# Optimization experiments

Hardware: AMD Instinct MI355X
Metric: run time of the kernel (lower is better)

The kernel has to match this reference:

```python
import jax, jax.numpy as jnp
import numpy as np

NUM_EXPERTS = 8
HIDDEN = 2048
INTER = 4096
TOKENS = 8192  # divisible by NUM_EXPERTS


def setup_inputs() -> dict:
    key = jax.random.key(0)
    k1, k2, k3 = jax.random.split(key, 3)
    hidden_states = jax.random.normal(k1, (TOKENS, HIDDEN), dtype=jnp.float32)
    gate_up_proj = jax.random.normal(k2, (NUM_EXPERTS, HIDDEN, 2 * INTER), dtype=jnp.float32) * 0.02
    down_proj = jax.random.normal(k3, (NUM_EXPERTS, INTER, HIDDEN), dtype=jnp.float32) * 0.02
    return {"hidden_states": hidden_states, "gate_up_proj": gate_up_proj, "down_proj": down_proj}


def reference(hidden_states, gate_up_proj, down_proj):
    E, H = gate_up_proj.shape[0], gate_up_proj.shape[1]
    x = hidden_states.reshape(E, -1, H)                      # (E, T/E, H)
    gate_up = jnp.einsum('eth,ehf->etf', x, gate_up_proj)    # (E, T/E, 2I)
    gate, up = jnp.split(gate_up, 2, axis=-1)
    acted = up * jax.nn.silu(gate)                           # (E, T/E, I)
    out = jnp.einsum('eti,eih->eth', acted, down_proj)       # (E, T/E, H)
    return out.reshape(-1, H)
```

## Files before the change

### kernel.cpp

```cpp
#include <hip/hip_runtime.h>


#define E_   8
#define H_   2048
#define I_   4096
#define T_   8192
#define TPE  1024

typedef __bf16 bf16x8 __attribute__((ext_vector_type(8)));
typedef float  f32x4  __attribute__((ext_vector_type(4)));

__device__ __forceinline__ unsigned short f2bf(float f) {
  union { float f; unsigned int u; } v; v.f = f;
  unsigned int u = v.u;
  u += 0x7FFFu + ((u >> 16) & 1u);
  return (unsigned short)(u >> 16);
}

__device__ __forceinline__ void async16(const void* g, void* l) {
  __builtin_amdgcn_global_load_lds(
      (__attribute__((address_space(1))) void*)(g),
      (__attribute__((address_space(3))) void*)(l), 16, 0, 0);
}

__global__ void convert_bf16(const float* __restrict__ src,
                             unsigned short* __restrict__ dst, long n) {
  long i = ((long)blockIdx.x * blockDim.x + threadIdx.x) * 4;
  const long stride = (long)gridDim.x * blockDim.x * 4;
  for (; i < n; i += stride) {
    const float4 v = *(const float4*)&src[i];
    ushort4 o;
    o.x = f2bf(v.x); o.y = f2bf(v.y); o.z = f2bf(v.z); o.w = f2bf(v.w);
    *(ushort4*)&dst[i] = o;
  }
}

__global__ void transpose_bf16(const float* __restrict__ src,
                               unsigned short* __restrict__ dst,
                               int K, int N) {
  __shared__ float tile[32][33];
  const long base = (long)blockIdx.z * (long)K * (long)N;
  src += base; dst += base;
  const int n0 = blockIdx.x * 32, k0 = blockIdx.y * 32;
  const int r  = threadIdx.x >> 3;
  const int c4 = (threadIdx.x & 7) * 4;

  const float4 v = *(const float4*)&src[(long)(k0 + r) * N + n0 + c4];
  tile[r][c4 + 0] = v.x; tile[r][c4 + 1] = v.y;
  tile[r][c4 + 2] = v.z; tile[r][c4 + 3] = v.w;
  __syncthreads();

  ushort4 o;
  o.x = f2bf(tile[c4 + 0][r]);
  o.y = f2bf(tile[c4 + 1][r]);
  o.z = f2bf(tile[c4 + 2][r]);
  o.w = f2bf(tile[c4 + 3][r]);
  *(ushort4*)&dst[(long)(n0 + r) * K + k0 + c4] = o;
}

__global__ void transpose_w1_perm(const float* __restrict__ src,
                                  unsigned short* __restrict__ dst) {
  __shared__ float tile[32][33];
  const long sbase = (long)blockIdx.z * (long)H_ * (2 * I_);
  const long dbase = (long)blockIdx.z * (long)(2 * I_) * H_;
  const int n0 = blockIdx.x * 32, k0 = blockIdx.y * 32;
  const int r  = threadIdx.x >> 3;
  const int c4 = (threadIdx.x & 7) * 4;

  const float4 v = *(const float4*)&src[sbase + (long)(k0 + r) * (2 * I_) + n0 + c4];
  tile[r][c4 + 0] = v.x; tile[r][c4 + 1] = v.y;
  tile[r][c4 + 2] = v.z; tile[r][c4 + 3] = v.w;
  __syncthreads();

  const int n = n0 + r;
  int np;
  if (n < I_) np = ((n >> 4) << 5) + (n & 15);
  else { const int j = n - I_; np = ((j >> 4) << 5) + 16 + (j & 15); }

  ushort4 o;
  o.x = f2bf(tile[c4 + 0][r]);
  o.y = f2bf(tile[c4 + 1][r]);
  o.z = f2bf(tile[c4 + 2][r]);
  o.w = f2bf(tile[c4 + 3][r]);
  *(ushort4*)&dst[dbase + (long)np * H_ + k0 + c4] = o;
}

template <int K, int NBN, bool SILU>
__global__ __launch_bounds__(512, 2)
void gemm_8ph(const unsigned short* __restrict__ Aall,
              const unsigned short* __restrict__ Ball,
              void* __restrict__ Cout,
              long sA, long sB, long sC) {
  extern __shared__ char smem[];
  constexpr int NT = K / 64;

  const int tid  = threadIdx.x;
  const int wave = tid >> 6;
  const int lane = tid & 63;
  const int lr   = lane & 15;
  const int lq   = lane >> 4;
  const int wid_m = wave >> 2;
  const int wid_n = wave & 3;

  const int nwg = gridDim.x;
  const int bid = blockIdx.x;
  const int wg  = (bid & 7) * (nwg >> 3) + (bid >> 3);
  const int mb  = wg & 3;
  const int tmp = wg >> 2;
  const int nb  = tmp % NBN;
  const int e   = tmp / NBN;

  const unsigned short* A = Aall + (long)e * sA + (long)(mb * 256) * K;
  const unsigned short* B = Ball + (long)e * sB + (long)(nb * 256) * K;

  const int stl  = tid >> 3;
  const int scol = ((tid & 7) ^ (stl & 7)) * 8;

  auto stageA = [&](int bi, int q, int kt) {
    const long col = (long)kt * 64 + scol;
    char* l0 = smem + bi * 32768 + q * 16384 + wave * 1024;
    async16(A + (long)(q * 64 + stl) * K + col,        l0);
    async16(A + (long)(128 + q * 64 + stl) * K + col,  l0 + 8192);
  };
  auto stageB = [&](int bi, int u, int kt) {
    const long col = (long)kt * 64 + scol;
    char* l0 = smem + 65536 + bi * 32768 + u * 16384 + wave * 1024;
    const int low = stl & 31;
    const int w0  = stl >> 5;
    async16(B + (long)((w0) * 64 + u * 32 + low) * K + col,     l0);
    async16(B + (long)((2 + w0) * 64 + u * 32 + low) * K + col, l0 + 8192);
  };

  const int ax0 = ((0 + lq) ^ (lr & 7)) * 16;
  const int ax1 = ((4 + lq) ^ (lr & 7)) * 16;

  f32x4 acc[8][4];
#pragma unroll
  for (int m = 0; m < 8; ++m)
#pragma unroll
    for (int n = 0; n < 4; ++n) acc[m][n] = (f32x4)0.0f;

  stageA(0, 0, 0);
  stageB(0, 1, 0);
  stageA(0, 1, 0);
  stageB(0, 0, 0);
  stageA(1, 0, NT > 1 ? 1 : 0);
  stageB(1, 1, NT > 1 ? 1 : 0);
  stageA(1, 1, NT > 1 ? 1 : 0);
  asm volatile("s_waitcnt vmcnt(6)" ::: "memory");
  __builtin_amdgcn_s_barrier();

#pragma unroll 1
  for (int t = 0; t < NT; ++t) {
    const int cur = t & 1;
    const char* LA = smem + cur * 32768;
    const char* LB = smem + 65536 + cur * 32768;
    const int t1v = (t + 1 < NT) ? t + 1 : NT - 1;
    const int t2v = (t + 2 < NT) ? t + 2 : NT - 1;
    const int bo  = cur ^ 1;

    bf16x8 a[4][2], b0[2][2], b1[2][2];

#pragma unroll
    for (int mf = 0; mf < 4; ++mf) {
      const int st = wid_m * 64 + mf * 16 + lr;
      a[mf][0] = *(const bf16x8*)(LA + st * 128 + ax0);
      a[mf][1] = *(const bf16x8*)(LA + st * 128 + ax1);
    }
#pragma unroll
    for (int nf = 0; nf < 2; ++nf) {
      const int st = wid_n * 32 + nf * 16 + lr;
      b0[nf][0] = *(const bf16x8*)(LB + st * 128 + ax0);
      b0[nf][1] = *(const bf16x8*)(LB + st * 128 + ax1);
    }
    stageB(bo, 0, t1v);
    __builtin_amdgcn_s_barrier();
    asm volatile("s_waitcnt lgkmcnt(0)" ::: "memory");
    __builtin_amdgcn_s_setprio(1);
#pragma unroll
    for (int mf = 0; mf < 4; ++mf)
#pragma unroll
      for (int nf = 0; nf < 2; ++nf) {
        acc[mf][nf] = __builtin_amdgcn_mfma_f32_16x16x32_bf16(a[mf][0], b0[nf][0], acc[mf][nf], 0, 0, 0);
        acc[mf][nf] = __builtin_amdgcn_mfma_f32_16x16x32_bf16(a[mf][1], b0[nf][1], acc[mf][nf], 0, 0, 0);
      }
    __builtin_amdgcn_s_setprio(0);
    __builtin_amdgcn_s_barrier();

#pragma unroll
    for (int nf = 0; nf < 2; ++nf) {
      const int st = 128 + wid_n * 32 + nf * 16 + lr;
      b1[nf][0] = *(const bf16x8*)(LB + st * 128 + ax0);
      b1[nf][1] = *(const bf16x8*)(LB + st * 128 + ax1);
    }
    stageA(cur, 0, t2v);
    __builtin_amdgcn_s_barrier();
    asm volatile("s_waitcnt lgkmcnt(0)" ::: "memory");
    __builtin_amdgcn_s_setprio(1);
#pragma unroll
    for (int mf = 0; mf < 4; ++mf)
#pragma unroll
      for (int nf = 0; nf < 2; ++nf) {
        acc[mf][2 + nf] = __builtin_amdgcn_mfma_f32_16x16x32_bf16(a[mf][0], b1[nf][0], acc[mf][2 + nf], 0, 0, 0);
        acc[mf][2 + nf] = __builtin_amdgcn_mfma_f32_16x16x32_bf16(a[mf][1], b1[nf][1], acc[mf][2 + nf], 0, 0, 0);
      }
    __builtin_amdgcn_s_setprio(0);
    __builtin_amdgcn_s_barrier();

#pragma unroll
    for (int mf = 0; mf < 4; ++mf) {
      const int st = 128 + wid_m * 64 + mf * 16 + lr;
      a[mf][0] = *(const bf16x8*)(LA + st * 128 + ax0);
      a[mf][1] = *(const bf16x8*)(LA + st * 128 + ax1);
    }
    stageB(cur, 1, t2v);
    __builtin_amdgcn_s_barrier();
    asm volatile("s_waitcnt lgkmcnt(0)" ::: "memory");
    __builtin_amdgcn_s_setprio(1);
#pragma unroll
    for (int mf = 0; mf < 4; ++mf)
#pragma unroll
      for (int nf = 0; nf < 2; ++nf) {
        acc[4 + mf][2 + nf] = __builtin_amdgcn_mfma_f32_16x16x32_bf16(a[mf][0], b1[nf][0], acc[4 + mf][2 + nf], 0, 0, 0);
        acc[4 + mf][2 + nf] = __builtin_amdgcn_mfma_f32_16x16x32_bf16(a[mf][1], b1[nf][1], acc[4 + mf][2 + nf], 0, 0, 0);
      }
    __builtin_amdgcn_s_setprio(0);
    __builtin_amdgcn_s_barrier();

    stageA(cur, 1, t2v);
    asm volatile("s_waitcnt vmcnt(6)" ::: "memory");
    __builtin_amdgcn_s_barrier();
    asm volatile("s_waitcnt lgkmcnt(0)" ::: "memory");
    __builtin_amdgcn_s_setprio(1);
#pragma unroll
    for (int mf = 0; mf < 4; ++mf)
#pragma unroll
      for (int nf = 0; nf < 2; ++nf) {
        acc[4 + mf][nf] = __builtin_amdgcn_mfma_f32_16x16x32_bf16(a[mf][0], b0[nf][0], acc[4 + mf][nf], 0, 0, 0);
        acc[4 + mf][nf] = __builtin_amdgcn_mfma_f32_16x16x32_bf16(a[mf][1], b0[nf][1], acc[4 + mf][nf], 0, 0, 0);
      }
    __builtin_amdgcn_s_setprio(0);
    __builtin_amdgcn_s_barrier();
  }

  if (SILU) {
    unsigned short* Cc = (unsigned short*)Cout + (long)e * sC;
    const int colbase = nb * 128 + wid_n * 32;
#pragma unroll
    for (int mf = 0; mf < 8; ++mf)
#pragma unroll
      for (int nfp = 0; nfp < 2; ++nfp)
#pragma unroll
        for (int rr = 0; rr < 4; ++rr) {
          const int row = mb * 256 + wid_m * 128 + mf * 16 + lq * 4 + rr;
          const int col = colbase + nfp * 16 + lr;
          const float g = acc[mf][nfp * 2][rr];
          const float u = acc[mf][nfp * 2 + 1][rr];
          Cc[(long)row * I_ + col] = f2bf(u * (g / (1.0f + __expf(-g))));
        }
  } else {
    float* Cc = (float*)Cout + (long)e * sC;
    const int colbase = nb * 256 + wid_n * 64;
#pragma unroll
    for (int mf = 0; mf < 8; ++mf)
#pragma unroll
      for (int nf = 0; nf < 4; ++nf)
#pragma unroll
        for (int rr = 0; rr < 4; ++rr) {
          const int row = mb * 256 + wid_m * 128 + mf * 16 + lq * 4 + rr;
          const int col = colbase + nf * 16 + lr;
          Cc[(long)row * H_ + col] = acc[mf][nf][rr];
        }
  }
}

extern "C" void kernel_launch(void* const* d_in, const int* in_sizes, int n_in,
                              void* d_out, int out_size, void* d_ws, size_t ws_size,
                              hipStream_t stream) {
  const float* hs = (const float*)d_in[0];
  const float* w1 = (const float*)d_in[1];
  const float* w2 = (const float*)d_in[2];
  float* out = (float*)d_out;
  char* ws = (char*)d_ws;

  const long HB_B  = (long)T_ * H_ * 2;
  const long ACT_B = (long)T_ * I_ * 2;
  const long W1T_B = (long)E_ * 2 * I_ * H_ * 2;
  const long W2T_B = (long)E_ * H_ * I_ * 2;
  if (ws_size < (size_t)(HB_B + ACT_B + W1T_B + W2T_B)) return;

  unsigned short* hiddenB = (unsigned short*)(ws);
  unsigned short* acted   = (unsigned short*)(ws + HB_B);
  unsigned short* W1t     = (unsigned short*)(ws + HB_B + ACT_B);
  unsigned short* W2t     = (unsigned short*)(ws + HB_B + ACT_B + W1T_B);

  hipLaunchKernelGGL(convert_bf16, dim3(2048), dim3(256), 0, stream,
                     hs, hiddenB, (long)T_ * H_);
  hipLaunchKernelGGL(transpose_w1_perm, dim3((2 * I_) / 32, H_ / 32, E_), dim3(256), 0, stream,
                     w1, W1t);
  hipLaunchKernelGGL(transpose_bf16, dim3(H_ / 32, I_ / 32, E_), dim3(256), 0, stream,
                     w2, W2t, I_, H_);

  hipLaunchKernelGGL((gemm_8ph<H_, 32, true>), dim3(1024), dim3(512), 131072, stream,
                     hiddenB, W1t, acted,
                     (long)TPE * H_, (long)2 * I_ * H_, (long)TPE * I_);
  hipLaunchKernelGGL((gemm_8ph<I_, 8, false>), dim3(256), dim3(512), 131072, stream,
                     acted, W2t, out,
                     (long)TPE * I_, (long)H_ * I_, (long)TPE * H_);
}
```

Measured before the change: 620.2 us.

## Fuse fp32 weight transpose and bf16 conversion into GEMM B-operand staging

Removes the separate weight transpose/convert kernels and their bf16 workspace. Each GEMM now reads fp32 weights straight from the original layout through registers, converts them to bf16 and writes the swizzled tile to LDS, with the gate/up interleave folded into the column mapping. This saves a full read and write pass over the large weight tensors. The cost is strided scalar global loads (one float per k-row per thread) in place of 16-byte async loads, plus more register and VALU work inside the main loop.

```diff
diff --git a/kernel.cpp b/kernel.cpp
--- a/kernel.cpp
+++ b/kernel.cpp
@@ -22,6 +22,11 @@
       (__attribute__((address_space(1))) void*)(g),
       (__attribute__((address_space(3))) void*)(l), 16, 0, 0);
 }
+
+#define SB0()    __builtin_amdgcn_sched_barrier(0)
+#define BAR()    __builtin_amdgcn_s_barrier()
+#define WAITLGKM() asm volatile("s_waitcnt lgkmcnt(0)" ::: "memory")
+#define WAITVM(n)  asm volatile("s_waitcnt vmcnt(" #n ")" ::: "memory")
 
 __global__ void convert_bf16(const float* __restrict__ src,
                              unsigned short* __restrict__ dst, long n) {
@@ -35,62 +40,12 @@
   }
 }
 
-__global__ void transpose_bf16(const float* __restrict__ src,
-                               unsigned short* __restrict__ dst,
-                               int K, int N) {
-  __shared__ float tile[32][33];
-  const long base = (long)blockIdx.z * (long)K * (long)N;
-  src += base; dst += base;
-  const int n0 = blockIdx.x * 32, k0 = blockIdx.y * 32;
-  const int r  = threadIdx.x >> 3;
-  const int c4 = (threadIdx.x & 7) * 4;
-
-  const float4 v = *(const float4*)&src[(long)(k0 + r) * N + n0 + c4];
-  tile[r][c4 + 0] = v.x; tile[r][c4 + 1] = v.y;
-  tile[r][c4 + 2] = v.z; tile[r][c4 + 3] = v.w;
-  __syncthreads();
-
-  ushort4 o;
-  o.x = f2bf(tile[c4 + 0][r]);
-  o.y = f2bf(tile[c4 + 1][r]);
-  o.z = f2bf(tile[c4 + 2][r]);
-  o.w = f2bf(tile[c4 + 3][r]);
-  *(ushort4*)&dst[(long)(n0 + r) * K + k0 + c4] = o;
-}
-
-__global__ void transpose_w1_perm(const float* __restrict__ src,
-                                  unsigned short* __restrict__ dst) {
-  __shared__ float tile[32][33];
-  const long sbase = (long)blockIdx.z * (long)H_ * (2 * I_);
-  const long dbase = (long)blockIdx.z * (long)(2 * I_) * H_;
-  const int n0 = blockIdx.x * 32, k0 = blockIdx.y * 32;
-  const int r  = threadIdx.x >> 3;
-  const int c4 = (threadIdx.x & 7) * 4;
-
-  const float4 v = *(const float4*)&src[sbase + (long)(k0 + r) * (2 * I_) + n0 + c4];
-  tile[r][c4 + 0] = v.x; tile[r][c4 + 1] = v.y;
-  tile[r][c4 + 2] = v.z; tile[r][c4 + 3] = v.w;
-  __syncthreads();
-
-  const int n = n0 + r;
-  int np;
-  if (n < I_) np = ((n >> 4) << 5) + (n & 15);
-  else { const int j = n - I_; np = ((j >> 4) << 5) + 16 + (j & 15); }
-
-  ushort4 o;
-  o.x = f2bf(tile[c4 + 0][r]);
-  o.y = f2bf(tile[c4 + 1][r]);
-  o.z = f2bf(tile[c4 + 2][r]);
-  o.w = f2bf(tile[c4 + 3][r]);
-  *(ushort4*)&dst[dbase + (long)np * H_ + k0 + c4] = o;
-}
-
-template <int K, int NBN, bool SILU>
+template <int K, int NBN, int LDB, bool SILU>
 __global__ __launch_bounds__(512, 2)
-void gemm_8ph(const unsigned short* __restrict__ Aall,
-              const unsigned short* __restrict__ Ball,
-              void* __restrict__ Cout,
-              long sA, long sB, long sC) {
+void gemm_fused(const unsigned short* __restrict__ Aall,
+                const float* __restrict__ Ball,
+                void* __restrict__ Cout,
+                long sA, long sB, long sC) {
   extern __shared__ char smem[];
   constexpr int NT = K / 64;
 
@@ -111,7 +66,7 @@
   const int e   = tmp / NBN;
 
   const unsigned short* A = Aall + (long)e * sA + (long)(mb * 256) * K;
-  const unsigned short* B = Ball + (long)e * sB + (long)(nb * 256) * K;
+  const float*          B = Ball + (long)e * sB;
 
   const int stl  = tid >> 3;
   const int scol = ((tid & 7) ^ (stl & 7)) * 8;
@@ -122,13 +77,46 @@
     async16(A + (long)(q * 64 + stl) * K + col,        l0);
     async16(A + (long)(128 + q * 64 + stl) * K + col,  l0 + 8192);
   };
-  auto stageB = [&](int bi, int u, int kt) {
-    const long col = (long)kt * 64 + scol;
-    char* l0 = smem + 65536 + bi * 32768 + u * 16384 + wave * 1024;
-    const int low = stl & 31;
-    const int w0  = stl >> 5;
-    async16(B + (long)((w0) * 64 + u * 32 + low) * K + col,     l0);
-    async16(B + (long)((2 + w0) * 64 + u * 32 + low) * K + col, l0 + 8192);
+
+  const int stB = tid & 255;
+  int colg;
+  {
+    const int b  = stB >> 7;
+    const int r  = stB & 127;
+    const int w  = r >> 5;
+    const int nf = (r >> 4) & 1;
+    const int l4 = stB & 15;
+    if (SILU) {
+      const int c = w * 32 + b * 16 + l4;
+      colg = nb * 128 + c + (nf ? I_ : 0);
+    } else {
+      colg = nb * 256 + w * 64 + (b * 2 + nf) * 16 + l4;
+    }
+  }
+  const float* Bp = B + colg;
+  const int koB = tid >> 8;
+
+  float bv[16];
+  auto loadB = [&](int g, int kt) {
+#pragma unroll
+    for (int uu = 0; uu < 2; ++uu) {
+      const int ko = (g * 2 + uu) * 2 + koB;
+      const long krow = (long)kt * 64 + ko * 8;
+#pragma unroll
+      for (int j = 0; j < 8; ++j)
+        bv[uu * 8 + j] = Bp[(krow + j) * (long)LDB];
+    }
+  };
+  auto writeB = [&](int bo, int g) {
+    char* LB = smem + 65536 + bo * 32768;
+#pragma unroll
+    for (int uu = 0; uu < 2; ++uu) {
+      const int ko = (g * 2 + uu) * 2 + koB;
+      bf16x8 pk;
+#pragma unroll
+      for (int j = 0; j < 8; ++j) pk[j] = (__bf16)bv[uu * 8 + j];
+      *(bf16x8*)(LB + stB * 128 + ((ko ^ (stB & 7)) * 16)) = pk;
+    }
   };
 
   const int ax0 = ((0 + lq) ^ (lr & 7)) * 16;
@@ -140,24 +128,30 @@
 #pragma unroll
     for (int n = 0; n < 4; ++n) acc[m][n] = (f32x4)0.0f;
 
+  const int t1p = (NT > 1) ? 1 : 0;
+  loadB(0, 0);
   stageA(0, 0, 0);
-  stageB(0, 1, 0);
   stageA(0, 1, 0);
-  stageB(0, 0, 0);
-  stageA(1, 0, NT > 1 ? 1 : 0);
-  stageB(1, 1, NT > 1 ? 1 : 0);
-  stageA(1, 1, NT > 1 ? 1 : 0);
-  asm volatile("s_waitcnt vmcnt(6)" ::: "memory");
-  __builtin_amdgcn_s_barrier();
+  SB0();
+  WAITVM(4);
+  writeB(0, 0);
+  loadB(1, 0);
+  stageA(1, 0, t1p);
+  stageA(1, 1, t1p);
+  SB0();
+  WAITVM(4);
+  writeB(0, 1);
+  WAITLGKM();
+  BAR();
 
 #pragma unroll 1
   for (int t = 0; t < NT; ++t) {
     const int cur = t & 1;
+    const int bo  = cur ^ 1;
     const char* LA = smem + cur * 32768;
     const char* LB = smem + 65536 + cur * 32768;
     const int t1v = (t + 1 < NT) ? t + 1 : NT - 1;
     const int t2v = (t + 2 < NT) ? t + 2 : NT - 1;
-    const int bo  = cur ^ 1;
 
     bf16x8 a[4][2], b0[2][2], b1[2][2];
 
@@ -173,9 +167,10 @@
       b0[nf][0] = *(const bf16x8*)(LB + st * 128 + ax0);
       b0[nf][1] = *(const bf16x8*)(LB + st * 128 + ax1);
     }
-    stageB(bo, 0, t1v);
-    __builtin_amdgcn_s_barrier();
-    asm volatile("s_waitcnt lgkmcnt(0)" ::: "memory");
+    loadB(0, t1v);
+    SB0();
+    BAR();
+    WAITLGKM();
     __builtin_amdgcn_s_setprio(1);
 #pragma unroll
     for (int mf = 0; mf < 4; ++mf)
@@ -185,7 +180,7 @@
         acc[mf][nf] = __builtin_amdgcn_mfma_f32_16x16x32_bf16(a[mf][1], b0[nf][1], acc[mf][nf], 0, 0, 0);
       }
     __builtin_amdgcn_s_setprio(0);
-    __builtin_amdgcn_s_barrier();
+    BAR();
 
 #pragma unroll
     for (int nf = 0; nf < 2; ++nf) {
@@ -194,8 +189,9 @@
       b1[nf][1] = *(const bf16x8*)(LB + st * 128 + ax1);
     }
     stageA(cur, 0, t2v);
-    __builtin_amdgcn_s_barrier();
-    asm volatile("s_waitcnt lgkmcnt(0)" ::: "memory");
+    SB0();
+    BAR();
+    WAITLGKM();
     __builtin_amdgcn_s_setprio(1);
 #pragma unroll
     for (int mf = 0; mf < 4; ++mf)
@@ -205,7 +201,7 @@
         acc[mf][2 + nf] = __builtin_amdgcn_mfma_f32_16x16x32_bf16(a[mf][1], b1[nf][1], acc[mf][2 + nf], 0, 0, 0);
       }
     __builtin_amdgcn_s_setprio(0);
-    __builtin_amdgcn_s_barrier();
+    BAR();
 
 #pragma unroll
     for (int mf = 0; mf < 4; ++mf) {
@@ -213,9 +209,12 @@
       a[mf][0] = *(const bf16x8*)(LA + st * 128 + ax0);
       a[mf][1] = *(const bf16x8*)(LA + st * 128 + ax1);
     }
-    stageB(cur, 1, t2v);
-    __builtin_amdgcn_s_barrier();
-    asm volatile("s_waitcnt lgkmcnt(0)" ::: "memory");
+    WAITVM(2);
+    writeB(bo, 0);
+    loadB(1, t1v);
+    SB0();
+    BAR();
+    WAITLGKM();
     __builtin_amdgcn_s_setprio(1);
 #pragma unroll
     for (int mf = 0; mf < 4; ++mf)
@@ -225,12 +224,14 @@
         acc[4 + mf][2 + nf] = __builtin_amdgcn_mfma_f32_16x16x32_bf16(a[mf][1], b1[nf][1], acc[4 + mf][2 + nf], 0, 0, 0);
       }
     __builtin_amdgcn_s_setprio(0);
-    __builtin_amdgcn_s_barrier();
+    BAR();
 
     stageA(cur, 1, t2v);
-    asm volatile("s_waitcnt vmcnt(6)" ::: "memory");
-    __builtin_amdgcn_s_barrier();
-    asm volatile("s_waitcnt lgkmcnt(0)" ::: "memory");
+    SB0();
+    WAITVM(2);
+    writeB(bo, 1);
+    WAITLGKM();
+    BAR();
     __builtin_amdgcn_s_setprio(1);
 #pragma unroll
     for (int mf = 0; mf < 4; ++mf)
@@ -240,36 +241,35 @@
         acc[4 + mf][nf] = __builtin_amdgcn_mfma_f32_16x16x32_bf16(a[mf][1], b0[nf][1], acc[4 + mf][nf], 0, 0, 0);
       }
     __builtin_amdgcn_s_setprio(0);
-    __builtin_amdgcn_s_barrier();
+    BAR();
   }
 
+  const int lqq = lane >> 4;
   if (SILU) {
     unsigned short* Cc = (unsigned short*)Cout + (long)e * sC;
-    const int colbase = nb * 128 + wid_n * 32;
 #pragma unroll
     for (int mf = 0; mf < 8; ++mf)
 #pragma unroll
-      for (int nfp = 0; nfp < 2; ++nfp)
+      for (int p = 0; p < 2; ++p)
 #pragma unroll
         for (int rr = 0; rr < 4; ++rr) {
-          const int row = mb * 256 + wid_m * 128 + mf * 16 + lq * 4 + rr;
-          const int col = colbase + nfp * 16 + lr;
-          const float g = acc[mf][nfp * 2][rr];
-          const float u = acc[mf][nfp * 2 + 1][rr];
+          const int row = mb * 256 + wid_m * 128 + mf * 16 + lqq * 4 + rr;
+          const int col = nb * 128 + wid_n * 32 + p * 16 + lr;
+          const float g = acc[mf][p * 2][rr];
+          const float u = acc[mf][p * 2 + 1][rr];
           Cc[(long)row * I_ + col] = f2bf(u * (g / (1.0f + __expf(-g))));
         }
   } else {
     float* Cc = (float*)Cout + (long)e * sC;
-    const int colbase = nb * 256 + wid_n * 64;
 #pragma unroll
     for (int mf = 0; mf < 8; ++mf)
 #pragma unroll
-      for (int nf = 0; nf < 4; ++nf)
+      for (int q = 0; q < 4; ++q)
 #pragma unroll
         for (int rr = 0; rr < 4; ++rr) {
-          const int row = mb * 256 + wid_m * 128 + mf * 16 + lq * 4 + rr;
-          const int col = colbase + nf * 16 + lr;
-          Cc[(long)row * H_ + col] = acc[mf][nf][rr];
+          const int row = mb * 256 + wid_m * 128 + mf * 16 + lqq * 4 + rr;
+          const int col = nb * 256 + wid_n * 64 + q * 16 + lr;
+          Cc[(long)row * H_ + col] = acc[mf][q][rr];
         }
   }
 }
@@ -285,26 +285,21 @@
 
   const long HB_B  = (long)T_ * H_ * 2;
   const long ACT_B = (long)T_ * I_ * 2;
-  const long W1T_B = (long)E_ * 2 * I_ * H_ * 2;
-  const long W2T_B = (long)E_ * H_ * I_ * 2;
-  if (ws_size < (size_t)(HB_B + ACT_B + W1T_B + W2T_B)) return;
+  if (ws_size < (size_t)(HB_B + ACT_B)) return;
 
   unsigned short* hiddenB = (unsigned short*)(ws);
   unsigned short* acted   = (unsigned short*)(ws + HB_B);
-  unsigned short* W1t     = (unsigned short*)(ws + HB_B + ACT_B);
-  unsigned short* W2t     = (unsigned short*)(ws + HB_B + ACT_B + W1T_B);
 
   hipLaunchKernelGGL(convert_bf16, dim3(2048), dim3(256), 0, stream,
                      hs, hiddenB, (long)T_ * H_);
-  hipLaunchKernelGGL(transpose_w1_perm, dim3((2 * I_) / 32, H_ / 32, E_), dim3(256), 0, stream,
-                     w1, W1t);
-  hipLaunchKernelGGL(transpose_bf16, dim3(H_ / 32, I_ / 32, E_), dim3(256), 0, stream,
-                     w2, W2t, I_, H_);
-
-  hipLaunchKernelGGL((gemm_8ph<H_, 32, true>), dim3(1024), dim3(512), 131072, stream,
-                     hiddenB, W1t, acted,
-                     (long)TPE * H_, (long)2 * I_ * H_, (long)TPE * I_);
-  hipLaunchKernelGGL((gemm_8ph<I_, 8, false>), dim3(256), dim3(512), 131072, stream,
-                     acted, W2t, out,
-                     (long)TPE * I_, (long)H_ * I_, (long)TPE * H_);
-}
+
+  hipLaunchKernelGGL((gemm_fused<H_, 32, 2 * I_, true>),
+                     dim3(1024), dim3(512), 131072, stream,
+                     hiddenB, w1, acted,
+                     (long)TPE * H_, (long)H_ * 2 * I_, (long)TPE * I_);
+
+  hipLaunchKernelGGL((gemm_fused<I_, 8, H_, false>),
+                     dim3(256), dim3(512), 131072, stream,
+                     acted, w2, out,
+                     (long)TPE * I_, (long)I_ * H_, (long)TPE * H_);
+}
```

After: 604.2 us. 1.03x faster.
